# Kernel optimization log

Hardware: AMD Instinct MI355X
Metric: run time of the kernel (lower is better)

The kernel has to match this reference:

```python
import jax, jax.numpy as jnp
import numpy as np
from jax import lax

B, MID, OUT, H, W = 16, 128, 512, 112, 112
EPS = 1e-5


def _conv(x, w, stride=1, pad=0, dil=1, groups=1):
    return lax.conv_general_dilated(
        x, w, window_strides=(stride, stride),
        padding=[(pad, pad), (pad, pad)], rhs_dilation=(dil, dil),
        feature_group_count=groups,
        dimension_numbers=('NCHW', 'OIHW', 'NCHW'))


def setup_inputs() -> dict:
    key = jax.random.key(0)
    ks = jax.random.split(key, 12)
    s = 0.05
    return {
        'x': jax.random.normal(ks[0], (B, 2 * MID, H, W), jnp.float32),
        # kernel_gen: Linear(mid, mid*9, bias=False) weight [mid*9, mid]
        'W_kg': jax.random.normal(ks[1], (MID * 9, MID), jnp.float32) * s,
        # global stream: depthwise 3x3 dil=2, then 1x1 conv, BN
        'gdw_w': jax.random.normal(ks[2], (MID, 1, 3, 3), jnp.float32) * s,
        'gdw_b': jax.random.normal(ks[3], (MID,), jnp.float32) * s,
        'gpw_w': jax.random.normal(ks[4], (MID, MID, 1, 1), jnp.float32) * s,
        'gpw_b': jax.random.normal(ks[5], (MID,), jnp.float32) * s,
        'bn1_g': jnp.ones((MID,), jnp.float32),
        'bn1_b': jnp.zeros((MID,), jnp.float32),
        'bn1_m': jax.random.normal(ks[6], (MID,), jnp.float32) * s,
        'bn1_v': jax.random.uniform(ks[7], (MID,), jnp.float32, 0.5, 1.5),
        # downsample: Conv2d(2*mid, out, 3, stride=2, pad=1), BN
        'ds_w': jax.random.normal(ks[8], (OUT, 2 * MID, 3, 3), jnp.float32) * s,
        'ds_b': jax.random.normal(ks[9], (OUT,), jnp.float32) * s,
        'bn2_g': jnp.ones((OUT,), jnp.float32),
        'bn2_b': jnp.zeros((OUT,), jnp.float32),
        'bn2_m': jax.random.normal(ks[10], (OUT,), jnp.float32) * s,
        'bn2_v': jax.random.uniform(ks[11], (OUT,), jnp.float32, 0.5, 1.5),
    }


def _bn(x, g, b, m, v):  # eval-mode BatchNorm2d
    inv = g / jnp.sqrt(v + EPS)
    return x * inv[None, :, None, None] + (b - m * inv)[None, :, None, None]


def reference(x, W_kg, gdw_w, gdw_b, gpw_w, gpw_b,
              bn1_g, bn1_b, bn1_m, bn1_v,
              ds_w, ds_b, bn2_g, bn2_b, bn2_m, bn2_v):
    local_in, global_in = jnp.split(x, 2, axis=1)  # [B,MID,H,W] each
    b, c, h, w = local_in.shape

    # local branch: pool -> linear+relu kernel-gen -> per-sample depthwise 3x3
    pooled = jnp.mean(local_in, axis=(2, 3))                  # [b,c]
    kernels = jax.nn.relu(pooled @ W_kg.T)                    # [b, c*9]
    kernels = kernels.reshape(b * c, 1, 3, 3)
    local_out = _conv(local_in.reshape(1, b * c, h, w), kernels,
                      pad=1, groups=b * c).reshape(b, c, h, w)

    # global branch: depthwise dil-2 conv -> 1x1 conv -> BN -> ReLU
    g = _conv(global_in, gdw_w, pad=2, dil=2, groups=c) + gdw_b[None, :, None, None]
    g = _conv(g, gpw_w) + gpw_b[None, :, None, None]
    g = jax.nn.relu(_bn(g, bn1_g, bn1_b, bn1_m, bn1_v))

    combined = jnp.concatenate([local_out, g], axis=1)        # [b,2c,h,w]
    out = _conv(combined, ds_w, stride=2, pad=1) + ds_b[None, :, None, None]
    out = jax.nn.relu(_bn(out, bn2_g, bn2_b, bn2_m, bn2_v))   # [b,OUT,h/2,w/2]
    return out
```

## Files before the change

kernel.cpp:

```cpp
#include <hip/hip_runtime.h>


#define DEVI static __device__ __forceinline__

using bf16x8 = __attribute__((ext_vector_type(8))) short;
using f32x4  = __attribute__((ext_vector_type(4))) float;
typedef unsigned short ushort_t;

constexpr int Bn = 16, MID = 128, CHN = 256, Hh = 112, Wn = 112;
constexpr int OHn = 56, OWn = 56, OCn = 512;
constexpr int HW  = Hh * Wn;
constexpr float EPSf = 1e-5f;

constexpr size_t C_I = 56 * 64;
constexpr size_t C_P = 4 * C_I;
constexpr size_t C_H = 2 * C_P;
constexpr size_t C_B = (size_t)Hh * C_H;

DEVI ushort_t f2b(float f) {
    unsigned u = __float_as_uint(f);
    return (ushort_t)((u + 0x7FFFu + ((u >> 16) & 1u)) >> 16);
}
DEVI float b2f(ushort_t s) { return __uint_as_float(((unsigned)s) << 16); }
DEVI int pack2(float a, float b) {
    return (int)f2b(a) | ((int)f2b(b) << 16);
}

DEVI void gl_lds16(const void* g, void* l) {
    __builtin_amdgcn_global_load_lds(
        (const __attribute__((address_space(1))) unsigned int*)g,
        (__attribute__((address_space(3))) unsigned int*)l, 16, 0, 0);
}

__global__ __launch_bounds__(256) void k_prep(
        const float* __restrict__ gpw_w, const float* __restrict__ gpw_b,
        const float* __restrict__ bn1g, const float* __restrict__ bn1b,
        const float* __restrict__ bn1m, const float* __restrict__ bn1v,
        const float* __restrict__ dsb,
        const float* __restrict__ bn2g, const float* __restrict__ bn2b,
        const float* __restrict__ bn2m, const float* __restrict__ bn2v,
        ushort_t* __restrict__ gpwbf,
        float* __restrict__ a1, float* __restrict__ b1,
        float* __restrict__ a2, float* __restrict__ b2,
        float* __restrict__ pooled) {
    int i = blockIdx.x * 256 + threadIdx.x;
    if (i < MID * MID) gpwbf[i] = f2b(gpw_w[i]);
    if (i < Bn * MID) pooled[i] = 0.f;
    if (i < OCn) {
        float inv = bn2g[i] / sqrtf(bn2v[i] + EPSf);
        a2[i] = inv;
        b2[i] = bn2b[i] + (dsb[i] - bn2m[i]) * inv;
    }
    if (i < MID) {
        float inv = bn1g[i] / sqrtf(bn1v[i] + EPSf);
        a1[i] = inv;
        b1[i] = bn1b[i] + (gpw_b[i] - bn1m[i]) * inv;
    }
}

__global__ __launch_bounds__(256) void k_wds(const float* __restrict__ dsw,
                                             ushort_t* __restrict__ wds2) {
    int d = blockIdx.x * 256 + threadIdx.x;
    int j = d & 63, oc = (d >> 6) & 511, kb = d >> 15;
    int khw = kb >> 2, icc = kb & 3;
    int ph = j >> 3, c = ph ^ (oc & 7);
    int ic = icc * 64 + c * 8 + (j & 7);
    wds2[d] = f2b(dsw[((size_t)oc * CHN + ic) * 9 + khw]);
}

__global__ __launch_bounds__(256) void k_kgen(const float* __restrict__ pooled,
                                              const float* __restrict__ wkg,
                                              float* __restrict__ kgen) {
    int idx = blockIdx.x * 256 + threadIdx.x;
    int b = idx / 1152, j = idx % 1152;
    int c = j & 127, tp = j >> 7;
    const float* pr = pooled + b * MID;
    const float* wr = wkg + (size_t)(c * 9 + tp) * MID;
    float s = 0.f;
#pragma unroll 8
    for (int i = 0; i < MID; i++) s += pr[i] * wr[i];
    kgen[idx] = fmaxf(s * (1.f / HW), 0.f);
}

__global__ __launch_bounds__(256) void k_xt(const float* __restrict__ x,
                                            ushort_t* __restrict__ xT,
                                            float* __restrict__ pooled) {
    __shared__ ushort_t tile[Wn * 264];
    int t = threadIdx.x;
    int bh = blockIdx.x;
    int b = bh / Hh, h = bh % Hh;
    const float* xp = x + ((size_t)b * CHN * Hh + h) * Wn;
    for (int idx = t; idx < CHN * 28; idx += 256) {
        int ch = idx / 28, q = idx % 28;
        float4 v = *(const float4*)(xp + (size_t)ch * HW + q * 4);
        int w = q * 4;
        tile[w * 264 + ch]       = f2b(v.x);
        tile[(w + 1) * 264 + ch] = f2b(v.y);
        tile[(w + 2) * 264 + ch] = f2b(v.z);
        tile[(w + 3) * 264 + ch] = f2b(v.w);
    }
    __syncthreads();
    int4* dst = (int4*)(xT + (size_t)bh * Wn * CHN);
    for (int q = t; q < Wn * CHN / 8; q += 256) {
        int w = q >> 5, c0 = (q & 31) << 3;
        dst[q] = *(const int4*)(tile + w * 264 + c0);
    }
    if (t < MID) {
        float s = 0.f;
        for (int w = 0; w < Wn; w++) s += b2f(tile[w * 264 + t]);
        atomicAdd(&pooled[b * MID + t], s);
    }
}

template <int DIL>
DEVI void dw_accum_row(const ushort_t* __restrict__ rp,
                       const float* __restrict__ wtab, int tb,
                       int c0, int wbase, float (&acc)[7][8]) {
    constexpr int NC = 7 + 2 * DIL;
    float wk[3][8];
#pragma unroll
    for (int dw = 0; dw < 3; dw++) {
        float4 lo = *(const float4*)&wtab[(tb + dw) * 128 + c0];
        float4 hi = *(const float4*)&wtab[(tb + dw) * 128 + c0 + 4];
        wk[dw][0] = lo.x; wk[dw][1] = lo.y; wk[dw][2] = lo.z; wk[dw][3] = lo.w;
        wk[dw][4] = hi.x; wk[dw][5] = hi.y; wk[dw][6] = hi.z; wk[dw][7] = hi.w;
    }
    int4 C[NC];
#pragma unroll
    for (int j = 0; j < NC; j++) {
        int w1 = wbase - DIL + j;
        int4 v = make_int4(0, 0, 0, 0);
        if ((unsigned)w1 < (unsigned)Wn)
            v = *(const int4*)(rp + (size_t)w1 * CHN);
        C[j] = v;
    }
#pragma unroll
    for (int j = 0; j < NC; j++) {
        float f[8];
        {
            unsigned u;
            u = (unsigned)C[j].x;
            f[0] = __uint_as_float(u << 16); f[1] = __uint_as_float(u & 0xffff0000u);
            u = (unsigned)C[j].y;
            f[2] = __uint_as_float(u << 16); f[3] = __uint_as_float(u & 0xffff0000u);
            u = (unsigned)C[j].z;
            f[4] = __uint_as_float(u << 16); f[5] = __uint_as_float(u & 0xffff0000u);
            u = (unsigned)C[j].w;
            f[6] = __uint_as_float(u << 16); f[7] = __uint_as_float(u & 0xffff0000u);
        }
#pragma unroll
        for (int dw = 0; dw < 3; dw++) {
            int i = j - dw * DIL;
            if (i >= 0 && i <= 6) {
#pragma unroll
                for (int k = 0; k < 8; k++) acc[i][k] += wk[dw][k] * f[k];
            }
        }
    }
}

__global__ __launch_bounds__(256, 3) void k_dw(
        const ushort_t* __restrict__ xT, const float* __restrict__ kgen,
        const float* __restrict__ gdw_w, const float* __restrict__ gdw_b,
        ushort_t* __restrict__ comb) {
    __shared__ float wtab[1152];
    int t = threadIdx.x;
    int h = blockIdx.x, by = blockIdx.y;
    int b = by >> 1, br = by & 1;
    if (br == 0) {
        const float4* src = (const float4*)(kgen + (size_t)b * 1152);
        float4* dstw = (float4*)wtab;
        dstw[t] = src[t];
        if (t < 32) dstw[256 + t] = src[256 + t];
    } else {
        for (int e4 = t; e4 < 288; e4 += 256) {
            float4 v = *(const float4*)(gdw_w + (size_t)e4 * 4);
            int e = e4 * 4;
            wtab[(e % 9) * 128 + e / 9]             = v.x;
            wtab[((e + 1) % 9) * 128 + (e + 1) / 9] = v.y;
            wtab[((e + 2) % 9) * 128 + (e + 2) / 9] = v.z;
            wtab[((e + 3) % 9) * 128 + (e + 3) / 9] = v.w;
        }
    }
    __syncthreads();
    int cg = t & 15, wl = t >> 4, c0 = cg << 3, wbase = 7 * wl;
    const ushort_t* xb = xT + (size_t)b * HW * CHN + (br ? MID : 0) + c0;
    float acc[7][8];
    if (br == 0) {
#pragma unroll
        for (int i = 0; i < 7; i++)
#pragma unroll
            for (int k = 0; k < 8; k++) acc[i][k] = 0.f;
#pragma unroll
        for (int dh = -1; dh <= 1; dh++) {
            int h1 = h + dh;
            if ((unsigned)h1 < (unsigned)Hh)
                dw_accum_row<1>(xb + (size_t)h1 * Wn * CHN, wtab,
                                (dh + 1) * 3, c0, wbase, acc);
        }
    } else {
        float4 b0 = *(const float4*)(gdw_b + c0);
        float4 b4 = *(const float4*)(gdw_b + c0 + 4);
#pragma unroll
        for (int i = 0; i < 7; i++) {
            acc[i][0] = b0.x; acc[i][1] = b0.y; acc[i][2] = b0.z; acc[i][3] = b0.w;
            acc[i][4] = b4.x; acc[i][5] = b4.y; acc[i][6] = b4.z; acc[i][7] = b4.w;
        }
#pragma unroll
        for (int dh = -1; dh <= 1; dh++) {
            int h1 = h + 2 * dh;
            if ((unsigned)h1 < (unsigned)Hh)
                dw_accum_row<2>(xb + (size_t)h1 * Wn * CHN, wtab,
                                (dh + 1) * 3, c0, wbase, acc);
        }
    }
    int gch = (br ? MID : 0) + c0;
    int icc = gch >> 6, cch = (gch & 63) >> 3;
#pragma unroll
    for (int i = 0; i < 7; i++) {
        int w = wbase + i;
        int4 O;
        O.x = pack2(acc[i][0], acc[i][1]);
        O.y = pack2(acc[i][2], acc[i][3]);
        O.z = pack2(acc[i][4], acc[i][5]);
        O.w = pack2(acc[i][6], acc[i][7]);
        int w2 = w >> 1, p = w & 1, ph = cch ^ (w2 & 7);
        *(int4*)(comb + (size_t)b * C_B + (size_t)h * C_H + p * C_P
                 + icc * C_I + w2 * 64 + ph * 8) = O;
    }
}

__global__ __launch_bounds__(256, 3) void k_pw(
        ushort_t* __restrict__ comb, const ushort_t* __restrict__ gpwbf,
        const float* __restrict__ a1, const float* __restrict__ b1) {
    __shared__ ushort_t pbuf[112 * 136];
    int t = threadIdx.x, lane = t & 63, wave = t >> 6;
    int h = blockIdx.x, b = blockIdx.y;
    const char* base = (const char*)(comb + (size_t)b * C_B + (size_t)h * C_H);
    for (int j = wave; j < 28; j += 4) {
        int s = j / 7, cc = j - s * 7;
        int p = s >> 1, ic = 2 + (s & 1);
        const char* src = base + ((size_t)p * C_P + (size_t)ic * C_I) * 2
                          + cc * 1024 + lane * 16;
        gl_lds16(src, (char*)pbuf + (size_t)s * 7168 + cc * 1024);
    }
    __syncthreads();
    int mrow = lane & 15, quad = lane >> 4;
    const short* gw = (const short*)gpwbf;
    f32x4 acc2[7][2] = {};
#pragma unroll
    for (int ks = 0; ks < 4; ks++) {
        bf16x8 bfr[2];
#pragma unroll
        for (int n = 0; n < 2; n++)
            bfr[n] = *(const bf16x8*)(gw + (size_t)(wave * 32 + n * 16 + mrow) * MID
                                         + ks * 32 + quad * 8);
        int kq = ks * 4 + quad;
#pragma unroll
        for (int m = 0; m < 7; m++) {
            int row = m * 16 + mrow;
            int p = (row >= 56) ? 1 : 0;
            int w2 = row - 56 * p;
            int slab = p * 2 + (kq >> 3);
            int ph = (kq & 7) ^ (w2 & 7);
            bf16x8 af = *(const bf16x8*)(pbuf + (size_t)slab * 3584
                                         + w2 * 64 + ph * 8);
#pragma unroll
            for (int n = 0; n < 2; n++)
                acc2[m][n] = __builtin_amdgcn_mfma_f32_16x16x32_bf16(
                    af, bfr[n], acc2[m][n], 0, 0, 0);
        }
    }
    __syncthreads();
#pragma unroll
    for (int m = 0; m < 7; m++)
#pragma unroll
        for (int n = 0; n < 2; n++) {
            int oc2 = wave * 32 + n * 16 + mrow;
            float al = a1[oc2], be = b1[oc2];
#pragma unroll
            for (int r = 0; r < 4; r++) {
                int px = m * 16 + quad * 4 + r;
                pbuf[px * 136 + oc2] = f2b(fmaxf(acc2[m][n][r] * al + be, 0.f));
            }
        }
    __syncthreads();
    int cg = t & 15, wl = t >> 4, c0 = cg << 3;
    for (int ws = 0; ws < 7; ws++) {
        int row = ws * 16 + wl;
        int p = (row >= 56) ? 1 : 0;
        int w2 = row - 56 * p;
        int4 v = *(const int4*)(pbuf + (size_t)row * 136 + c0);
        int gch = MID + c0;
        int icc = gch >> 6, cch = (gch & 63) >> 3, ph = cch ^ (w2 & 7);
        *(int4*)(comb + (size_t)b * C_B + (size_t)h * C_H + (size_t)p * C_P
                 + icc * C_I + w2 * 64 + ph * 8) = v;
    }
}

__global__ __launch_bounds__(256) void k_ds(
        const ushort_t* __restrict__ comb, const ushort_t* __restrict__ wds2,
        const float* __restrict__ a2, const float* __restrict__ b2,
        float* __restrict__ out) {
    __shared__ ushort_t lA[128 * 64];
    __shared__ ushort_t lB[128 * 64];
    int t = threadIdx.x, lane = t & 63, wave = t >> 6;
    int g = blockIdx.x;
    int xcd = g & 7, s = g >> 3;
    int octile = s & 3, pl = s >> 2;
    int pair = xcd * 56 + pl;
    int bb = pair / 28, ohp = pair % 28;
    int oh0 = ohp * 2, oc0 = octile * 128;
    int mrow = lane & 15, quad = lane >> 4;
    int wm = wave & 1, wn = wave >> 1;
    int ak = mrow & 7;

    f32x4 acc[4][4] = {};
    for (int kt = 0; kt < 36; kt++) {
        int khw = kt >> 2, icc = kt & 3;
        int kh = khw / 3, kw = khw - kh * 3;
        int p = (kw == 1) ? 0 : 1;
        bool zh0 = (oh0 == 0) && (kh == 0);
        int ldsShift = (kw == 0) ? 128 : 0;
        __syncthreads();
        if (zh0) {
            int4 z = {0, 0, 0, 0};
            *(int4*)(lB + t * 8) = z;
            *(int4*)(lB + 2048 + t * 8) = z;
        }
        if (kw == 0 && t < 16) {
            int4 z = {0, 0, 0, 0};
            *(int4*)(lB + (t >> 3) * 4096 + (t & 7) * 8) = z;
        }
        const char* asrc = (const char*)wds2
            + ((size_t)kt * 32768 + (size_t)oc0 * 64) * 2 + lane * 16;
#pragma unroll
        for (int i = 0; i < 4; i++) {
            int j = wave * 4 + i;
            gl_lds16(asrc + j * 1024, (char*)lA + j * 1024);
        }
        for (int j = wave; j < 14; j += 4) {
            int osub = (j >= 7) ? 1 : 0, jj = j - osub * 7;
            if (zh0 && osub == 0) continue;
            int r = 2 * oh0 + 2 * osub + kh - 1;
            const char* bsrc = (const char*)comb
                + ((size_t)bb * C_B + (size_t)r * C_H + (size_t)p * C_P
                   + (size_t)icc * C_I) * 2 + jj * 1024 + lane * 16;
            gl_lds16(bsrc, (char*)lB + osub * 8192 + ldsShift + jj * 1024);
        }
        __syncthreads();
        int bk = (mrow + ((kw == 0) ? 7 : 0)) & 7;
#pragma unroll
        for (int ks = 0; ks < 2; ks++) {
            bf16x8 af[4], bf[4];
#pragma unroll
            for (int m = 0; m < 4; m++) {
                int row = wm * 64 + m * 16 + mrow;
                int ph = (ks * 4 + quad) ^ ak;
                af[m] = *(const bf16x8*)(lA + row * 64 + ph * 8);
            }
#pragma unroll
            for (int n = 0; n < 4; n++) {
                int nr = wn * 64 + n * 16 + mrow;
                int ph = (ks * 4 + quad) ^ bk;
                bf[n] = *(const bf16x8*)(lB + nr * 64 + ph * 8);
            }
#pragma unroll
            for (int m = 0; m < 4; m++)
#pragma unroll
                for (int n = 0; n < 4; n++)
                    acc[m][n] = __builtin_amdgcn_mfma_f32_16x16x32_bf16(
                        af[m], bf[n], acc[m][n], 0, 0, 0);
        }
    }
#pragma unroll
    for (int m = 0; m < 4; m++) {
#pragma unroll
        for (int r4 = 0; r4 < 4; r4++) {
            int oc = oc0 + wm * 64 + m * 16 + quad * 4 + r4;
            float al = a2[oc], be = b2[oc];
#pragma unroll
            for (int n = 0; n < 4; n++) {
                int nr = wn * 64 + n * 16 + mrow;
                int osub = nr >> 6, ow = nr & 63;
                if (ow < OWn) {
                    float v = fmaxf(acc[m][n][r4] * al + be, 0.f);
                    out[((size_t)(bb * OCn + oc) * OHn + (oh0 + osub)) * OWn + ow] = v;
                }
            }
        }
    }
}

extern "C" void kernel_launch(void* const* d_in, const int* in_sizes, int n_in,
                              void* d_out, int out_size, void* d_ws, size_t ws_size,
                              hipStream_t stream) {
    const float* x     = (const float*)d_in[0];
    const float* wkg   = (const float*)d_in[1];
    const float* gdw_w = (const float*)d_in[2];
    const float* gdw_b = (const float*)d_in[3];
    const float* gpw_w = (const float*)d_in[4];
    const float* gpw_b = (const float*)d_in[5];
    const float* bn1g  = (const float*)d_in[6];
    const float* bn1b  = (const float*)d_in[7];
    const float* bn1m  = (const float*)d_in[8];
    const float* bn1v  = (const float*)d_in[9];
    const float* dsw   = (const float*)d_in[10];
    const float* dsb   = (const float*)d_in[11];
    const float* bn2g  = (const float*)d_in[12];
    const float* bn2b  = (const float*)d_in[13];
    const float* bn2m  = (const float*)d_in[14];
    const float* bn2v  = (const float*)d_in[15];

    char* ws = (char*)d_ws;
    float*    pooled = (float*)(ws + 0);
    float*    kgen   = (float*)(ws + 8192);
    float*    a1     = (float*)(ws + 81920);
    float*    b1     = (float*)(ws + 82432);
    float*    a2     = (float*)(ws + 82944);
    float*    b2     = (float*)(ws + 84992);
    ushort_t* gpwbf  = (ushort_t*)(ws + 87040);
    ushort_t* wds2   = (ushort_t*)(ws + 119808);
    ushort_t* comb   = (ushort_t*)(ws + 2479104);
    ushort_t* xT  = (ushort_t*)d_out;
    float*    out = (float*)d_out;

    k_prep<<<64, 256, 0, stream>>>(gpw_w, gpw_b, bn1g, bn1b, bn1m, bn1v,
                                   dsb, bn2g, bn2b, bn2m, bn2v,
                                   gpwbf, a1, b1, a2, b2, pooled);
    k_wds <<<4608, 256, 0, stream>>>(dsw, wds2);
    k_xt  <<<1792, 256, 0, stream>>>(x, xT, pooled);
    k_kgen<<<72, 256, 0, stream>>>(pooled, wkg, kgen);
    k_dw  <<<dim3(Hh, Bn * 2), 256, 0, stream>>>(xT, kgen, gdw_w, gdw_b, comb);
    k_pw  <<<dim3(Hh, Bn), 256, 0, stream>>>(comb, gpwbf, a1, b1);
    k_ds  <<<1792, 256, 0, stream>>>(comb, wds2, a2, b2, out);
}
```

Baseline: 344.4 us.

## Double-buffer activation tiles in LDS and load weights directly to registers in k_ds

The downsample conv GEMM now double-buffers the activation (B) tile in LDS, staging the next k-step while the current one is computed, and drops one barrier per iteration. Weight fragments are read straight from global memory into registers instead of going through LDS, so the weight layout loses its XOR swizzle. Launch bounds now request two blocks per SM. This aims to hide global-to-LDS latency behind the MFMA work, at the cost of uncoalesced, latency-exposed weight loads and more register pressure.

```diff
diff --git a/kernel.cpp b/kernel.cpp
--- a/kernel.cpp
+++ b/kernel.cpp
@@ -61,10 +61,9 @@
 __global__ __launch_bounds__(256) void k_wds(const float* __restrict__ dsw,
                                              ushort_t* __restrict__ wds2) {
     int d = blockIdx.x * 256 + threadIdx.x;
-    int j = d & 63, oc = (d >> 6) & 511, kb = d >> 15;
-    int khw = kb >> 2, icc = kb & 3;
-    int ph = j >> 3, c = ph ^ (oc & 7);
-    int ic = icc * 64 + c * 8 + (j & 7);
+    int kk = d & 63, oc = (d >> 6) & 511, kt = d >> 15;
+    int khw = kt >> 2, icc = kt & 3;
+    int ic = icc * 64 + kk;
     wds2[d] = f2b(dsw[((size_t)oc * CHN + ic) * 9 + khw]);
 }
 
@@ -298,12 +297,11 @@
     }
 }
 
-__global__ __launch_bounds__(256) void k_ds(
+__global__ __launch_bounds__(256, 2) void k_ds(
         const ushort_t* __restrict__ comb, const ushort_t* __restrict__ wds2,
         const float* __restrict__ a2, const float* __restrict__ b2,
         float* __restrict__ out) {
-    __shared__ ushort_t lA[128 * 64];
-    __shared__ ushort_t lB[128 * 64];
+    __shared__ ushort_t lB[2][128 * 64];
     int t = threadIdx.x, lane = t & 63, wave = t >> 6;
     int g = blockIdx.x;
     int xcd = g & 7, s = g >> 3;
@@ -313,31 +311,24 @@
     int oh0 = ohp * 2, oc0 = octile * 128;
     int mrow = lane & 15, quad = lane >> 4;
     int wm = wave & 1, wn = wave >> 1;
-    int ak = mrow & 7;
-
-    f32x4 acc[4][4] = {};
-    for (int kt = 0; kt < 36; kt++) {
-        int khw = kt >> 2, icc = kt & 3;
+
+    const ushort_t* Abase = wds2 + (size_t)(oc0 + wm * 64 + mrow) * 64 + quad * 8;
+
+    auto STAGE = [&](int ktn, int nb) {
+        int khw = ktn >> 2, icc = ktn & 3;
         int kh = khw / 3, kw = khw - kh * 3;
         int p = (kw == 1) ? 0 : 1;
         bool zh0 = (oh0 == 0) && (kh == 0);
         int ldsShift = (kw == 0) ? 128 : 0;
-        __syncthreads();
+        ushort_t* Bb = (ushort_t*)lB[nb];
         if (zh0) {
             int4 z = {0, 0, 0, 0};
-            *(int4*)(lB + t * 8) = z;
-            *(int4*)(lB + 2048 + t * 8) = z;
+            *(int4*)(Bb + t * 8) = z;
+            *(int4*)(Bb + 2048 + t * 8) = z;
         }
         if (kw == 0 && t < 16) {
             int4 z = {0, 0, 0, 0};
-            *(int4*)(lB + (t >> 3) * 4096 + (t & 7) * 8) = z;
-        }
-        const char* asrc = (const char*)wds2
-            + ((size_t)kt * 32768 + (size_t)oc0 * 64) * 2 + lane * 16;
-#pragma unroll
-        for (int i = 0; i < 4; i++) {
-            int j = wave * 4 + i;
-            gl_lds16(asrc + j * 1024, (char*)lA + j * 1024);
+            *(int4*)(Bb + (t >> 3) * 4096 + (t & 7) * 8) = z;
         }
         for (int j = wave; j < 14; j += 4) {
             int osub = (j >= 7) ? 1 : 0, jj = j - osub * 7;
@@ -346,32 +337,44 @@
             const char* bsrc = (const char*)comb
                 + ((size_t)bb * C_B + (size_t)r * C_H + (size_t)p * C_P
                    + (size_t)icc * C_I) * 2 + jj * 1024 + lane * 16;
-            gl_lds16(bsrc, (char*)lB + osub * 8192 + ldsShift + jj * 1024);
-        }
-        __syncthreads();
+            gl_lds16(bsrc, (char*)Bb + osub * 8192 + ldsShift + jj * 1024);
+        }
+    };
+
+    f32x4 acc[4][4] = {};
+    STAGE(0, 0);
+    __syncthreads();
+    for (int kt = 0; kt < 36; kt++) {
+        int cur = kt & 1;
+        bf16x8 af[2][4];
+        const ushort_t* Ak = Abase + (size_t)kt * 32768;
+#pragma unroll
+        for (int ks = 0; ks < 2; ks++)
+#pragma unroll
+            for (int m = 0; m < 4; m++)
+                af[ks][m] = *(const bf16x8*)(Ak + m * 1024 + ks * 32);
+        if (kt < 35) STAGE(kt + 1, cur ^ 1);
+        const ushort_t* Bb = (const ushort_t*)lB[cur];
+        int khw = kt >> 2;
+        int kh = khw / 3, kw = khw - kh * 3;
         int bk = (mrow + ((kw == 0) ? 7 : 0)) & 7;
 #pragma unroll
         for (int ks = 0; ks < 2; ks++) {
-            bf16x8 af[4], bf[4];
-#pragma unroll
-            for (int m = 0; m < 4; m++) {
-                int row = wm * 64 + m * 16 + mrow;
-                int ph = (ks * 4 + quad) ^ ak;
-                af[m] = *(const bf16x8*)(lA + row * 64 + ph * 8);
-            }
+            bf16x8 bf[4];
 #pragma unroll
             for (int n = 0; n < 4; n++) {
                 int nr = wn * 64 + n * 16 + mrow;
                 int ph = (ks * 4 + quad) ^ bk;
-                bf[n] = *(const bf16x8*)(lB + nr * 64 + ph * 8);
+                bf[n] = *(const bf16x8*)(Bb + nr * 64 + ph * 8);
             }
 #pragma unroll
             for (int m = 0; m < 4; m++)
 #pragma unroll
                 for (int n = 0; n < 4; n++)
                     acc[m][n] = __builtin_amdgcn_mfma_f32_16x16x32_bf16(
-                        af[m], bf[n], acc[m][n], 0, 0, 0);
-        }
+                        af[ks][m], bf[n], acc[m][n], 0, 0, 0);
+        }
+        if (kt < 35) __syncthreads();
     }
 #pragma unroll
     for (int m = 0; m < 4; m++) {
```

New measurement: 485.7 us. 41.0% more time.
